# Kernel tuning notes

Hardware: AMD Instinct MI355X
Metric: run time of the kernel (lower is better)

The kernel has to match this reference:

```python
import jax, jax.numpy as jnp
import numpy as np

E = 640000   # n_edges
D = 128      # feature_dim
N = 40000    # n_dst_nodes


def setup_inputs() -> dict:
    key = jax.random.key(0)
    k1, k2, k3 = jax.random.split(key, 3)
    src_emb = jax.random.normal(k1, (E, D), dtype=jnp.float32)
    dst_idx = jax.random.randint(k2, (E,), 0, N, dtype=jnp.int64)
    # nn.Linear default init scale ~ 1/sqrt(fan_in)
    W = jax.random.normal(k3, (D, D), dtype=jnp.float32) / jnp.sqrt(jnp.float32(D))
    b = jnp.zeros((D,), dtype=jnp.float32)
    return {"src_emb": src_emb, "W": W, "b": b, "dst_idx": dst_idx, "n_nodes": N}


def reference(src_emb, W, b, dst_idx, n_nodes):
    # msg_e = relu(Linear(src_emb))  -- per-edge messages [E, D]
    msg = jax.nn.relu(jnp.einsum("ed,fd->ef", src_emb, W) + b)
    # update_all(copy_edge, max) == segment max over destination nodes [N, D]
    h_node = jax.ops.segment_max(msg, dst_idx, num_segments=n_nodes)
    return h_node
```

## Files before the change

kernel.cpp:

```cpp
#include <hip/hip_runtime.h>
#include <hip/hip_bf16.h>

#define E_EDGES 640000
#define DIM     128
#define N_NODES 40000

typedef __bf16 bf16x8 __attribute__((ext_vector_type(8)));
typedef float  floatx4 __attribute__((ext_vector_type(4)));

#define WS_WSW     0
#define WS_COUNTS  32768
#define WS_OFFSETS 196608
#define WS_CURSOR  360448
#define WS_SORTED  524288

__global__ void prep_kernel(const float* __restrict__ W,
                            __bf16* __restrict__ Wsw,
                            int* __restrict__ counts,
                            int* __restrict__ out_i) {
    int tid = blockIdx.x * blockDim.x + threadIdx.x;
    if (tid < N_NODES * DIM) out_i[tid] = 0xFF800000;
    if (tid < N_NODES) counts[tid] = 0;
    if (tid < 2048) {
        int lane = tid & 63;
        int kb   = (tid >> 6) & 3;
        int nb   = tid >> 8;
        int f    = nb * 16 + (lane & 15);
        int k0   = kb * 32 + ((lane >> 4) & 3) * 8;
        const float* wrow = W + f * DIM + k0;
        __bf16* o = Wsw + tid * 8;
#pragma unroll
        for (int j = 0; j < 8; ++j) o[j] = (__bf16)wrow[j];
    }
}

__global__ void hist_kernel(const int* __restrict__ dst, int* __restrict__ counts) {
    int e = blockIdx.x * blockDim.x + threadIdx.x;
    if (e < E_EDGES) atomicAdd(&counts[dst[e]], 1);
}

#define SCAN_T 1024
__global__ __launch_bounds__(SCAN_T)
void scan_kernel(const int* __restrict__ counts,
                 int* __restrict__ offsets,
                 int* __restrict__ cursor) {
    __shared__ int sm[SCAN_T];
    __shared__ int s_carry;
    int tid = threadIdx.x;
    if (tid == 0) s_carry = 0;
    __syncthreads();
    for (int base = 0; base < N_NODES; base += SCAN_T) {
        int i = base + tid;
        int x = (i < N_NODES) ? counts[i] : 0;
        sm[tid] = x;
        __syncthreads();
#pragma unroll
        for (int off = 1; off < SCAN_T; off <<= 1) {
            int v = (tid >= off) ? sm[tid - off] : 0;
            __syncthreads();
            sm[tid] += v;
            __syncthreads();
        }
        int carry = s_carry;
        int incl  = sm[tid];
        if (i < N_NODES) {
            int excl = incl - x + carry;
            offsets[i] = excl;
            cursor[i]  = excl;
        }
        __syncthreads();
        if (tid == SCAN_T - 1) s_carry = carry + incl;
        __syncthreads();
    }
    if (tid == 0) offsets[N_NODES] = s_carry;
}

__global__ void scatter_kernel(const int* __restrict__ dst,
                               int* __restrict__ cursor,
                               int* __restrict__ sorted) {
    int e = blockIdx.x * blockDim.x + threadIdx.x;
    if (e < E_EDGES) {
        int pos = atomicAdd(&cursor[dst[e]], 1);
        sorted[pos] = e;
    }
}

__global__ __launch_bounds__(256)
void gemm_csr_kernel(const float* __restrict__ src,
                     const __bf16* __restrict__ Wsw,
                     const float* __restrict__ bias,
                     const int* __restrict__ offsets,
                     const int* __restrict__ sorted,
                     float* __restrict__ out) {
    const int lane = threadIdx.x & 63;
    const int wave = threadIdx.x >> 6;
    const int node = blockIdx.x * 4 + wave;
    if (node >= N_NODES) return;
    const int q = lane >> 4;
    const int n = lane & 15;

    const int s = offsets[node];
    const int e = offsets[node + 1];
    if (s == e) return;

    const bf16x8* Wf = (const bf16x8*)Wsw;

    float cmax[8];
#pragma unroll
    for (int nb = 0; nb < 8; ++nb) cmax[nb] = -3.0e38f;

    for (int t = s; t < e; t += 16) {
        int ei  = t + n;
        int eid = sorted[ei < e ? ei : e - 1];
        const float* arow = src + (size_t)eid * DIM + q * 8;

        floatx4 acc[8];
#pragma unroll
        for (int nb = 0; nb < 8; ++nb) acc[nb] = (floatx4)(0.0f);

#pragma unroll
        for (int kb = 0; kb < 4; ++kb) {
            float4 a0 = *(const float4*)(arow + kb * 32);
            float4 a1 = *(const float4*)(arow + kb * 32 + 4);
            bf16x8 af;
            af[0] = (__bf16)a0.x; af[1] = (__bf16)a0.y;
            af[2] = (__bf16)a0.z; af[3] = (__bf16)a0.w;
            af[4] = (__bf16)a1.x; af[5] = (__bf16)a1.y;
            af[6] = (__bf16)a1.z; af[7] = (__bf16)a1.w;
#pragma unroll
            for (int nb = 0; nb < 8; ++nb) {
                bf16x8 bf = Wf[(nb * 4 + kb) * 64 + lane];
                acc[nb] = __builtin_amdgcn_mfma_f32_16x16x32_bf16(af, bf, acc[nb], 0, 0, 0);
            }
        }
#pragma unroll
        for (int nb = 0; nb < 8; ++nb) {
            float m01 = acc[nb][0] > acc[nb][1] ? acc[nb][0] : acc[nb][1];
            float m23 = acc[nb][2] > acc[nb][3] ? acc[nb][2] : acc[nb][3];
            float m = m01 > m23 ? m01 : m23;
            cmax[nb] = cmax[nb] > m ? cmax[nb] : m;
        }
    }

#pragma unroll
    for (int nb = 0; nb < 8; ++nb) {
        float v = cmax[nb];
        float o = __shfl_xor(v, 16);
        v = v > o ? v : o;
        o = __shfl_xor(v, 32);
        v = v > o ? v : o;
        if (q == 0) {
            int col = nb * 16 + n;
            float r = v + bias[col];
            out[(size_t)node * DIM + col] = r > 0.0f ? r : 0.0f;
        }
    }
}

extern "C" void kernel_launch(void* const* d_in, const int* in_sizes, int n_in,
                              void* d_out, int out_size, void* d_ws, size_t ws_size,
                              hipStream_t stream) {
    const float* src  = (const float*)d_in[0];
    const float* W    = (const float*)d_in[1];
    const float* bias = (const float*)d_in[2];
    const int*   dst  = (const int*)d_in[3];

    char* ws = (char*)d_ws;
    __bf16* Wsw     = (__bf16*)(ws + WS_WSW);
    int*    counts  = (int*)(ws + WS_COUNTS);
    int*    offsets = (int*)(ws + WS_OFFSETS);
    int*    cursor  = (int*)(ws + WS_CURSOR);
    int*    sorted  = (int*)(ws + WS_SORTED);
    float*  out     = (float*)d_out;

    prep_kernel<<<(N_NODES * DIM + 255) / 256, 256, 0, stream>>>(W, Wsw, counts, (int*)d_out);
    hist_kernel<<<(E_EDGES + 255) / 256, 256, 0, stream>>>(dst, counts);
    scan_kernel<<<1, SCAN_T, 0, stream>>>(counts, offsets, cursor);
    scatter_kernel<<<(E_EDGES + 255) / 256, 256, 0, stream>>>(dst, cursor, sorted);
    gemm_csr_kernel<<<(N_NODES + 3) / 4, 256, 0, stream>>>(src, Wsw, bias, offsets, sorted, out);
}
```

Measured before the change: 697.4 us.

## Compute edge messages densely, scatter bf16 to sorted order, then segment-max

Replaces the single-block scan with a three-stage multi-block scan. When the workspace is large enough, it computes the GEMM over edges in their original order, so src rows are read coalesced instead of gathered. The bf16 messages are written to their CSR-sorted positions via an inverse permutation, and a separate segment-max kernel reduces contiguous rows per node. This adds a write and read of a bf16 message buffer (about 164 MB) plus an extra launch in exchange for coalesced input reads and full-tile MFMA use. It also rounds messages to bf16 before the max.

```diff
diff --git a/kernel.cpp b/kernel.cpp
--- a/kernel.cpp
+++ b/kernel.cpp
@@ -8,11 +8,14 @@
 typedef __bf16 bf16x8 __attribute__((ext_vector_type(8)));
 typedef float  floatx4 __attribute__((ext_vector_type(4)));
 
-#define WS_WSW     0
-#define WS_COUNTS  32768
-#define WS_OFFSETS 196608
-#define WS_CURSOR  360448
-#define WS_SORTED  524288
+#define WS_WSW      0u
+#define WS_COUNTS   32768u
+#define WS_OFFSETS  196608u
+#define WS_CURSOR   360448u
+#define WS_PARTIALS 520448u
+#define WS_INV      524288u
+#define WS_MSG      3145728u
+#define WS_NEEDED   (WS_MSG + (size_t)E_EDGES * DIM * 2)
 
 __global__ void prep_kernel(const float* __restrict__ W,
                             __bf16* __restrict__ Wsw,
@@ -39,49 +42,186 @@
     if (e < E_EDGES) atomicAdd(&counts[dst[e]], 1);
 }
 
-#define SCAN_T 1024
-__global__ __launch_bounds__(SCAN_T)
-void scan_kernel(const int* __restrict__ counts,
-                 int* __restrict__ offsets,
-                 int* __restrict__ cursor) {
-    __shared__ int sm[SCAN_T];
-    __shared__ int s_carry;
-    int tid = threadIdx.x;
-    if (tid == 0) s_carry = 0;
+#define SB 256
+#define SE 4
+__global__ __launch_bounds__(SB)
+void scan1_kernel(const int* __restrict__ counts,
+                  int* __restrict__ loc,
+                  int* __restrict__ partials) {
+    __shared__ int sm[SB];
+    int b = blockIdx.x, tid = threadIdx.x;
+    int base = b * SB * SE + tid * SE;
+    int v[SE], s = 0;
+#pragma unroll
+    for (int j = 0; j < SE; ++j) {
+        int i = base + j;
+        v[j] = (i < N_NODES) ? counts[i] : 0;
+        s += v[j];
+    }
+    sm[tid] = s;
     __syncthreads();
-    for (int base = 0; base < N_NODES; base += SCAN_T) {
-        int i = base + tid;
-        int x = (i < N_NODES) ? counts[i] : 0;
-        sm[tid] = x;
+#pragma unroll
+    for (int off = 1; off < SB; off <<= 1) {
+        int t = (tid >= off) ? sm[tid - off] : 0;
         __syncthreads();
-#pragma unroll
-        for (int off = 1; off < SCAN_T; off <<= 1) {
-            int v = (tid >= off) ? sm[tid - off] : 0;
-            __syncthreads();
-            sm[tid] += v;
-            __syncthreads();
-        }
-        int carry = s_carry;
-        int incl  = sm[tid];
-        if (i < N_NODES) {
-            int excl = incl - x + carry;
-            offsets[i] = excl;
-            cursor[i]  = excl;
-        }
+        sm[tid] += t;
         __syncthreads();
-        if (tid == SCAN_T - 1) s_carry = carry + incl;
-        __syncthreads();
-    }
-    if (tid == 0) offsets[N_NODES] = s_carry;
-}
-
-__global__ void scatter_kernel(const int* __restrict__ dst,
-                               int* __restrict__ cursor,
-                               int* __restrict__ sorted) {
+    }
+    int excl = sm[tid] - s;
+    if (tid == SB - 1) partials[b] = sm[tid];
+    int run = excl;
+#pragma unroll
+    for (int j = 0; j < SE; ++j) {
+        int i = base + j;
+        if (i < N_NODES) loc[i] = run;
+        run += v[j];
+    }
+}
+
+__global__ void scan2_kernel(int* __restrict__ partials, int nblocks) {
+    int lane = threadIdx.x & 63;
+    int v = (lane < nblocks) ? partials[lane] : 0;
+    int orig = v;
+#pragma unroll
+    for (int off = 1; off < 64; off <<= 1) {
+        int o = __shfl_up(v, off);
+        if (lane >= off) v += o;
+    }
+    if (lane < nblocks) partials[lane] = v - orig;
+}
+
+__global__ void scan3_kernel(int* __restrict__ offsets,
+                             const int* __restrict__ partials,
+                             int* __restrict__ cursor) {
+    int i = blockIdx.x * blockDim.x + threadIdx.x;
+    if (i < N_NODES) {
+        int o = offsets[i] + partials[i / (SB * SE)];
+        offsets[i] = o;
+        cursor[i]  = o;
+    }
+    if (i == 0) offsets[N_NODES] = E_EDGES;
+}
+
+__global__ void scatter_inv_kernel(const int* __restrict__ dst,
+                                   int* __restrict__ cursor,
+                                   int* __restrict__ inv) {
+    int e = blockIdx.x * blockDim.x + threadIdx.x;
+    if (e < E_EDGES) inv[e] = atomicAdd(&cursor[dst[e]], 1);
+}
+
+__global__ void scatter_sorted_kernel(const int* __restrict__ dst,
+                                      int* __restrict__ cursor,
+                                      int* __restrict__ sorted) {
     int e = blockIdx.x * blockDim.x + threadIdx.x;
     if (e < E_EDGES) {
         int pos = atomicAdd(&cursor[dst[e]], 1);
         sorted[pos] = e;
+    }
+}
+
+__global__ __launch_bounds__(256)
+void gemm_scatter_kernel(const float* __restrict__ src,
+                         const __bf16* __restrict__ Wsw,
+                         const int* __restrict__ inv,
+                         __bf16* __restrict__ msg) {
+    const int lane = threadIdx.x & 63;
+    const int wave = threadIdx.x >> 6;
+    const int q    = lane >> 4;
+    const int n    = lane & 15;
+    const int eb   = blockIdx.x * 64 + wave * 16;
+
+    int pos[4];
+#pragma unroll
+    for (int r = 0; r < 4; ++r) pos[r] = inv[eb + q * 4 + r];
+
+    floatx4 acc[8];
+#pragma unroll
+    for (int nb = 0; nb < 8; ++nb) acc[nb] = (floatx4)(0.0f);
+
+    const float* arow = src + (size_t)(eb + n) * DIM + q * 8;
+    const bf16x8* Wf = (const bf16x8*)Wsw;
+
+#pragma unroll
+    for (int kb = 0; kb < 4; ++kb) {
+        float4 a0 = *(const float4*)(arow + kb * 32);
+        float4 a1 = *(const float4*)(arow + kb * 32 + 4);
+        bf16x8 af;
+        af[0] = (__bf16)a0.x; af[1] = (__bf16)a0.y;
+        af[2] = (__bf16)a0.z; af[3] = (__bf16)a0.w;
+        af[4] = (__bf16)a1.x; af[5] = (__bf16)a1.y;
+        af[6] = (__bf16)a1.z; af[7] = (__bf16)a1.w;
+#pragma unroll
+        for (int nb = 0; nb < 8; ++nb) {
+            bf16x8 bf = Wf[(nb * 4 + kb) * 64 + lane];
+            acc[nb] = __builtin_amdgcn_mfma_f32_16x16x32_bf16(af, bf, acc[nb], 0, 0, 0);
+        }
+    }
+
+#pragma unroll
+    for (int r = 0; r < 4; ++r) {
+        bf16x8 o;
+#pragma unroll
+        for (int nb = 0; nb < 8; ++nb) o[nb] = (__bf16)acc[nb][r];
+        *(bf16x8*)(msg + (size_t)pos[r] * DIM + n * 8) = o;
+    }
+}
+
+__global__ __launch_bounds__(256)
+void segmax_kernel(const __bf16* __restrict__ msg,
+                   const float* __restrict__ bias,
+                   const int* __restrict__ offsets,
+                   float* __restrict__ out) {
+    const int lane = threadIdx.x & 63;
+    const int wave = threadIdx.x >> 6;
+    const int node = blockIdx.x * 4 + wave;
+    if (node >= N_NODES) return;
+    const int rg = lane >> 4;
+    const int n  = lane & 15;
+
+    const int s = offsets[node];
+    const int e = offsets[node + 1];
+    if (s == e) return;
+
+    float vm[8];
+#pragma unroll
+    for (int j = 0; j < 8; ++j) vm[j] = -3.0e38f;
+
+    int t = s + rg;
+    for (; t + 4 < e; t += 8) {
+        bf16x8 m0 = *(const bf16x8*)(msg + (size_t)t * DIM + n * 8);
+        bf16x8 m1 = *(const bf16x8*)(msg + (size_t)(t + 4) * DIM + n * 8);
+#pragma unroll
+        for (int j = 0; j < 8; ++j) {
+            float f0 = (float)m0[j], f1 = (float)m1[j];
+            float f = f0 > f1 ? f0 : f1;
+            vm[j] = vm[j] > f ? vm[j] : f;
+        }
+    }
+    if (t < e) {
+        bf16x8 m0 = *(const bf16x8*)(msg + (size_t)t * DIM + n * 8);
+#pragma unroll
+        for (int j = 0; j < 8; ++j) {
+            float f0 = (float)m0[j];
+            vm[j] = vm[j] > f0 ? vm[j] : f0;
+        }
+    }
+
+#pragma unroll
+    for (int j = 0; j < 8; ++j) {
+        float v = vm[j];
+        float o = __shfl_xor(v, 16);
+        v = v > o ? v : o;
+        o = __shfl_xor(v, 32);
+        v = v > o ? v : o;
+        vm[j] = v;
+    }
+    if (rg == 0) {
+#pragma unroll
+        for (int j = 0; j < 8; ++j) {
+            int col = j * 16 + n;
+            float r = vm[j] + bias[col];
+            out[(size_t)node * DIM + col] = r > 0.0f ? r : 0.0f;
+        }
     }
 }
 
@@ -104,7 +244,6 @@
     if (s == e) return;
 
     const bf16x8* Wf = (const bf16x8*)Wsw;
-
     float cmax[8];
 #pragma unroll
     for (int nb = 0; nb < 8; ++nb) cmax[nb] = -3.0e38f;
@@ -113,11 +252,9 @@
         int ei  = t + n;
         int eid = sorted[ei < e ? ei : e - 1];
         const float* arow = src + (size_t)eid * DIM + q * 8;
-
         floatx4 acc[8];
 #pragma unroll
         for (int nb = 0; nb < 8; ++nb) acc[nb] = (floatx4)(0.0f);
-
 #pragma unroll
         for (int kb = 0; kb < 4; ++kb) {
             float4 a0 = *(const float4*)(arow + kb * 32);
@@ -141,7 +278,6 @@
             cmax[nb] = cmax[nb] > m ? cmax[nb] : m;
         }
     }
-
 #pragma unroll
     for (int nb = 0; nb < 8; ++nb) {
         float v = cmax[nb];
@@ -166,16 +302,29 @@
     const int*   dst  = (const int*)d_in[3];
 
     char* ws = (char*)d_ws;
-    __bf16* Wsw     = (__bf16*)(ws + WS_WSW);
-    int*    counts  = (int*)(ws + WS_COUNTS);
-    int*    offsets = (int*)(ws + WS_OFFSETS);
-    int*    cursor  = (int*)(ws + WS_CURSOR);
-    int*    sorted  = (int*)(ws + WS_SORTED);
-    float*  out     = (float*)d_out;
+    __bf16* Wsw      = (__bf16*)(ws + WS_WSW);
+    int*    counts   = (int*)(ws + WS_COUNTS);
+    int*    offsets  = (int*)(ws + WS_OFFSETS);
+    int*    cursor   = (int*)(ws + WS_CURSOR);
+    int*    partials = (int*)(ws + WS_PARTIALS);
+    int*    inv      = (int*)(ws + WS_INV);
+    __bf16* msg      = (__bf16*)(ws + WS_MSG);
+    float*  out      = (float*)d_out;
+
+    const int scan_blocks = (N_NODES + SB * SE - 1) / (SB * SE);
 
     prep_kernel<<<(N_NODES * DIM + 255) / 256, 256, 0, stream>>>(W, Wsw, counts, (int*)d_out);
     hist_kernel<<<(E_EDGES + 255) / 256, 256, 0, stream>>>(dst, counts);
-    scan_kernel<<<1, SCAN_T, 0, stream>>>(counts, offsets, cursor);
-    scatter_kernel<<<(E_EDGES + 255) / 256, 256, 0, stream>>>(dst, cursor, sorted);
-    gemm_csr_kernel<<<(N_NODES + 3) / 4, 256, 0, stream>>>(src, Wsw, bias, offsets, sorted, out);
-}
+    scan1_kernel<<<scan_blocks, SB, 0, stream>>>(counts, offsets, partials);
+    scan2_kernel<<<1, 64, 0, stream>>>(partials, scan_blocks);
+    scan3_kernel<<<(N_NODES + 255) / 256, 256, 0, stream>>>(offsets, partials, cursor);
+
+    if (ws_size >= WS_NEEDED) {
+        scatter_inv_kernel<<<(E_EDGES + 255) / 256, 256, 0, stream>>>(dst, cursor, inv);
+        gemm_scatter_kernel<<<E_EDGES / 64, 256, 0, stream>>>(src, Wsw, inv, msg);
+        segmax_kernel<<<(N_NODES + 3) / 4, 256, 0, stream>>>(msg, bias, offsets, out);
+    } else {
+        scatter_sorted_kernel<<<(E_EDGES + 255) / 256, 256, 0, stream>>>(dst, cursor, inv);
+        gemm_csr_kernel<<<(N_NODES + 3) / 4, 256, 0, stream>>>(src, Wsw, bias, offsets, inv, out);
+    }
+}
```

Result: faster. 578.9 us (-17.0%).
